# Optimization experiments

Measured on AMD Instinct MI355X. Metric: run time of the kernel, lower is better.

## Reference

```python
import jax, jax.numpy as jnp
import numpy as np

N_NODES = 50000
N_EDGES = 400000
F_IN = 128
HID = 64
HEADS = 8
N_CLASSES = 16
NEG_SLOPE = 0.2  # PyG GATConv default negative_slope


def _glorot(key, shape):
    fan_in, fan_out = shape[0], shape[-1]
    lim = jnp.sqrt(6.0 / (fan_in + fan_out))
    return jax.random.uniform(key, shape, jnp.float32, -lim, lim)


def setup_inputs() -> dict:
    key = jax.random.key(0)
    ks = jax.random.split(key, 16)
    x = jax.random.normal(ks[0], (N_NODES, F_IN), jnp.float32)
    edge_index = jax.random.randint(ks[1], (2, N_EDGES), 0, N_NODES, jnp.int64)
    # layer 0: F_IN -> HEADS*HID (concat)
    W0 = _glorot(ks[2], (F_IN, HEADS * HID))
    a_s0 = _glorot(ks[3], (HEADS, HID))
    a_d0 = _glorot(ks[4], (HEADS, HID))
    b0 = jnp.zeros((HEADS * HID,), jnp.float32)
    # layer 1: HEADS*HID -> HEADS*HID (concat)
    W1 = _glorot(ks[5], (HEADS * HID, HEADS * HID))
    a_s1 = _glorot(ks[6], (HEADS, HID))
    a_d1 = _glorot(ks[7], (HEADS, HID))
    b1 = jnp.zeros((HEADS * HID,), jnp.float32)
    # final layer: HEADS*HID -> N_CLASSES, heads=1, concat=False (mean over heads)
    W2 = _glorot(ks[8], (HEADS * HID, 1 * N_CLASSES))
    a_s2 = _glorot(ks[9], (1, N_CLASSES))
    a_d2 = _glorot(ks[10], (1, N_CLASSES))
    b2 = jnp.zeros((N_CLASSES,), jnp.float32)
    return {"x": x, "edge_index": edge_index,
            "W0": W0, "a_s0": a_s0, "a_d0": a_d0, "b0": b0,
            "W1": W1, "a_s1": a_s1, "a_d1": a_d1, "b1": b1,
            "W2": W2, "a_s2": a_s2, "a_d2": a_d2, "b2": b2}


def gat_conv(x, src, dst, W, a_src, a_dst, b, num_nodes, concat):
    """One PyG-style GATConv (self-loops already in src/dst).
    x: [N, F_in]; W: [F_in, H*C]; a_src/a_dst: [H, C]; b: [H*C] or [C]."""
    H, C = a_src.shape
    h = (x @ W).reshape(num_nodes, H, C)                    # [N,H,C]
    al_s = jnp.einsum('nhc,hc->nh', h, a_src)               # [N,H]
    al_d = jnp.einsum('nhc,hc->nh', h, a_dst)               # [N,H]
    e = jax.nn.leaky_relu(al_s[src] + al_d[dst], NEG_SLOPE) # [E,H]
    # scatter-softmax over incoming edges of each destination node
    m = jax.ops.segment_max(e, dst, num_segments=num_nodes)  # [N,H]
    ex = jnp.exp(e - m[dst])
    denom = jax.ops.segment_sum(ex, dst, num_segments=num_nodes)
    alpha = ex / denom[dst]                                  # [E,H]
    out = jax.ops.segment_sum(alpha[:, :, None] * h[src], dst,
                              num_segments=num_nodes)        # [N,H,C]
    if concat:
        return out.reshape(num_nodes, H * C) + b
    return out.mean(axis=1) + b


def reference(x, edge_index, W0, a_s0, a_d0, b0, W1, a_s1, a_d1, b1,
              W2, a_s2, a_d2, b2):
    N = x.shape[0]
    # PyG GATConv adds self-loops by default
    loops = jnp.arange(N, dtype=edge_index.dtype)
    src = jnp.concatenate([edge_index[0], loops])
    dst = jnp.concatenate([edge_index[1], loops])
    h = gat_conv(x, src, dst, W0, a_s0, a_d0, b0, N, concat=True)
    h = jax.nn.elu(h)  # dropout is identity in eval mode
    h = gat_conv(h, src, dst, W1, a_s1, a_d1, b1, N, concat=True)
    h = jax.nn.elu(h)
    return gat_conv(h, src, dst, W2, a_s2, a_d2, b2, N, concat=False)
```

## Files before the change

kernel.cpp:

```cpp
#include <hip/hip_runtime.h>

#define N_NODES 50000
#define N_EDGES 400000
#define E_TOT   450000
#define NEG 0.2f
#define NB_SCAN ((N_NODES + 255) / 256)
#define MAXD 64

typedef unsigned short ushort_t;
typedef __attribute__((ext_vector_type(8))) _Float16 half8;
typedef __attribute__((ext_vector_type(4))) float  f32x4;
typedef __attribute__((ext_vector_type(8))) unsigned short ushort8;

__device__ __forceinline__ ushort_t f2h(float f){
    _Float16 h = (_Float16)f;
    union { _Float16 h; ushort_t u; } v; v.h = h; return v.u;
}
__device__ __forceinline__ float h_lo(unsigned u){
    union { unsigned u; _Float16 h[2]; } v; v.u = u; return (float)v.h[0];
}
__device__ __forceinline__ float h_hi(unsigned u){
    union { unsigned u; _Float16 h[2]; } v; v.u = u; return (float)v.h[1];
}
__device__ __forceinline__ void gload_lds16(const void* g, void* l){
    __builtin_amdgcn_global_load_lds((const __attribute__((address_space(1))) void*)g,
                                     (__attribute__((address_space(3))) void*)l, 16, 0, 0);
}
__device__ __forceinline__ int wave_incl_scan(int v, int lane){
    #pragma unroll
    for(int off = 1; off < 64; off <<= 1){
        int t = __shfl_up(v, off, 64);
        if(lane >= off) v += t;
    }
    return v;
}


__global__ void count_deg(const int* __restrict__ ei, int* __restrict__ deg){
    int e = blockIdx.x*256 + threadIdx.x;
    if(e >= E_TOT) return;
    int dst = (e < N_EDGES) ? ei[N_EDGES + e] : (e - N_EDGES);
    atomicAdd(&deg[dst], 1);
}

__global__ void deg_block_sum(const int* __restrict__ deg, int* __restrict__ bsum){
    int i = blockIdx.x*256 + threadIdx.x;
    int lane = threadIdx.x & 63, wave = threadIdx.x >> 6;
    int v = (i < N_NODES) ? deg[i] : 0;
    #pragma unroll
    for(int off = 1; off < 64; off <<= 1) v += __shfl_xor(v, off, 64);
    __shared__ int sw[4];
    if(lane == 0) sw[wave] = v;
    __syncthreads();
    if(threadIdx.x == 0) bsum[blockIdx.x] = sw[0] + sw[1] + sw[2] + sw[3];
}

__global__ void scan_apply(const int* __restrict__ bsum,
                           int* __restrict__ dw, int* __restrict__ rowptr){
    __shared__ int soff;
    __shared__ int sw[4];
    int i = blockIdx.x*256 + threadIdx.x;
    int lane = threadIdx.x & 63, wave = threadIdx.x >> 6;
    if(wave == 0){
        int s = 0;
        for(int j = lane; j < (int)blockIdx.x; j += 64) s += bsum[j];
        #pragma unroll
        for(int off = 1; off < 64; off <<= 1) s += __shfl_xor(s, off, 64);
        if(lane == 0) soff = s;
    }
    int v = (i < N_NODES) ? dw[i] : 0;
    int incl = wave_incl_scan(v, lane);
    if(lane == 63) sw[wave] = incl;
    __syncthreads();
    int add = soff;
    for(int w = 0; w < wave; w++) add += sw[w];
    int excl = incl - v + add;
    if(i < N_NODES){ rowptr[i] = excl; dw[i] = excl; }
    if(i == N_NODES-1) rowptr[N_NODES] = excl + v;
}

__global__ void scatter_edges(const int* __restrict__ ei, int* __restrict__ wofs,
                              int* __restrict__ csr){
    int e = blockIdx.x*256 + threadIdx.x;
    if(e >= E_TOT) return;
    int src, dst;
    if(e < N_EDGES){ src = ei[e]; dst = ei[N_EDGES + e]; }
    else { src = dst = e - N_EDGES; }
    int pos = atomicAdd(&wofs[dst], 1);
    csr[pos] = src;
}


__global__ void cvt_all(const float* __restrict__ x, const float* __restrict__ W0,
                        const float* __restrict__ W1, const float* __restrict__ W2,
                        ushort_t* __restrict__ xbf, ushort_t* __restrict__ W0t,
                        ushort_t* __restrict__ W1t, ushort_t* __restrict__ W2t,
                        int* __restrict__ wofs){
    int i = blockIdx.x*256 + threadIdx.x;
    if(i < N_NODES*128) xbf[i] = f2h(x[i]);
    if(i < 512*128){ int n = i >> 7, k = i & 127; W0t[i] = f2h(W0[(size_t)k*512 + n]); }
    if(i < 512*512){ int n = i >> 9, k = i & 511; W1t[i] = f2h(W1[(size_t)k*512 + n]); }
    if(i < 16*512){ int n = i >> 9, k = i & 511; W2t[i] = f2h(W2[(size_t)k*16 + n]); }
    if(i < N_NODES) wofs[i] = 0;
}


template<int K>
__global__ __launch_bounds__(256) void gemm_bt(const ushort_t* __restrict__ A,
                                               const ushort_t* __restrict__ Bt,
                                               ushort_t* __restrict__ Cb,
                                               const float* __restrict__ a_s,
                                               const float* __restrict__ a_d,
                                               float* __restrict__ als,
                                               float* __restrict__ ald, int M){
    __shared__ ushort_t As[128*32];
    __shared__ ushort_t Bs[128*32];
    int tid  = threadIdx.x;
    int wave = tid >> 6, lane = tid & 63;
    int wm = wave & 1, wn = wave >> 1;
    int row0 = blockIdx.y * 128;
    int col0 = blockIdx.x * 128;

    f32x4 acc[4][4] = {};

    int lrow = lane >> 2;
    int lchk = (lane & 3) * 8;

    for(int kt = 0; kt < K; kt += 32){
        #pragma unroll
        for(int s = 0; s < 2; s++){
            int seg = wave*2 + s;
            int ar = row0 + seg*16 + lrow;
            ar = ar < M ? ar : M-1;
            gload_lds16(A  + (size_t)ar*K + kt + lchk, As + seg*512);
            int br = col0 + seg*16 + lrow;
            gload_lds16(Bt + (size_t)br*K + kt + lchk, Bs + seg*512);
        }
        __syncthreads();

        half8 a[4], b[4];
        int fm = lane & 15, fq = (lane >> 4) * 8;
        #pragma unroll
        for(int t = 0; t < 4; t++){
            a[t] = *(const half8*)&As[(wm*64 + t*16 + fm)*32 + fq];
            b[t] = *(const half8*)&Bs[(wn*64 + t*16 + fm)*32 + fq];
        }
        #pragma unroll
        for(int i = 0; i < 4; i++)
            #pragma unroll
            for(int j = 0; j < 4; j++)
                acc[i][j] = __builtin_amdgcn_mfma_f32_16x16x32_f16(a[i], b[j], acc[i][j], 0, 0, 0);
        __syncthreads();
    }

    int cm = (lane >> 4) * 4, cn = lane & 15;
    int head = (col0 + wn*64) >> 6;
    float as_[4], ad_[4];
    #pragma unroll
    for(int j = 0; j < 4; j++){
        int c = head*64 + cn + j*16;
        as_[j] = a_s[c]; ad_[j] = a_d[c];
    }
    #pragma unroll
    for(int i = 0; i < 4; i++){
        #pragma unroll
        for(int p = 0; p < 4; p++){
            int r = row0 + wm*64 + i*16 + cm + p;
            float ps = 0.f, pd = 0.f;
            if(r < M){
                ushort_t* cp = &Cb[(size_t)r*512 + col0 + wn*64 + cn];
                #pragma unroll
                for(int j = 0; j < 4; j++){
                    float v = acc[i][j][p];
                    cp[j*16] = f2h(v);
                    ps += v*as_[j]; pd += v*ad_[j];
                }
            }
            #pragma unroll
            for(int off = 1; off < 16; off <<= 1){
                ps += __shfl_xor(ps, off);
                pd += __shfl_xor(pd, off);
            }
            if(cn == 0 && r < M){ als[r*8 + head] = ps; ald[r*8 + head] = pd; }
        }
    }
}


__global__ __launch_bounds__(256, 4) void attn_agg(const ushort_t* __restrict__ h,
        const float* __restrict__ als, const float* __restrict__ ald,
        const int* __restrict__ rowptr, const int* __restrict__ csr,
        const float* __restrict__ bias, ushort_t* __restrict__ out){
    __shared__ float sm[4][8], sd[4][8];
    __shared__ float sex[4][MAXD][8];
    int wv = threadIdx.x >> 6, lane = threadIdx.x & 63;
    int n = blockIdx.x*4 + wv;
    int start = rowptr[n], end = rowptr[n+1];

    int cnt = end - start;
    int nmain = cnt < MAXD ? cnt : MAXD;
    int mend = start + nmain;
    int last = mend - 1;

    uint4 pp[8];
    #pragma unroll
    for(int k = 0; k < 8; k++){
        int j = start + k;
        int s = csr[j <= last ? j : last];
        pp[k] = *(const uint4*)&h[(size_t)s*512 + lane*8];
    }

    int hd = lane & 7, e8 = lane >> 3;
    float aldv = ald[n*8 + hd];
    float lmax = -1e30f;
    for(int idx = start + e8; idx < end; idx += 8){
        int e = idx - start;
        int src = csr[idx];
        float v = als[src*8 + hd] + aldv;
        v = v > 0.f ? v : NEG*v;
        if(e < MAXD) sex[wv][e][hd] = v;
        lmax = fmaxf(lmax, v);
    }
    for(int off = 8; off < 64; off <<= 1) lmax = fmaxf(lmax, __shfl_xor(lmax, off));
    float lsum = 0.f;
    for(int idx = start + e8; idx < end; idx += 8){
        int e = idx - start;
        float v;
        if(e < MAXD) v = sex[wv][e][hd];
        else { int src = csr[idx]; v = als[src*8 + hd] + aldv; v = v > 0.f ? v : NEG*v; }
        float ex = __expf(v - lmax);
        if(e < MAXD) sex[wv][e][hd] = ex;
        lsum += ex;
    }
    for(int off = 8; off < 64; off <<= 1) lsum += __shfl_xor(lsum, off);
    if(lane < 8){ sm[wv][hd] = lmax; sd[wv][hd] = 1.f / lsum; }
    __syncthreads();

    int head = lane >> 3;
    float inv = sd[wv][head];
    float acc[8] = {};

    int idx = start;
    for(;;){
        float ee[8];
        #pragma unroll
        for(int k = 0; k < 8; k++){
            int j = idx + k;
            ee[k] = (j < mend) ? sex[wv][j-start][head] : 0.f;
        }
        int nidx = idx + 8;
        bool more = nidx < mend;
        uint4 np[8];
        if(more){
            #pragma unroll
            for(int k = 0; k < 8; k++){
                int j = nidx + k;
                int s = csr[j <= last ? j : last];
                np[k] = *(const uint4*)&h[(size_t)s*512 + lane*8];
            }
        }
        #pragma unroll
        for(int k = 0; k < 8; k++){
            acc[0] += ee[k]*h_lo(pp[k].x); acc[1] += ee[k]*h_hi(pp[k].x);
            acc[2] += ee[k]*h_lo(pp[k].y); acc[3] += ee[k]*h_hi(pp[k].y);
            acc[4] += ee[k]*h_lo(pp[k].z); acc[5] += ee[k]*h_hi(pp[k].z);
            acc[6] += ee[k]*h_lo(pp[k].w); acc[7] += ee[k]*h_hi(pp[k].w);
        }
        if(!more) break;
        #pragma unroll
        for(int k = 0; k < 8; k++) pp[k] = np[k];
        idx = nidx;
    }

    if(mend < end){
        float m = sm[wv][head];
        float aldn = ald[n*8 + head];
        for(int ix = mend; ix < end; ix++){
            int src = csr[ix];
            float v = als[src*8 + head] + aldn;
            v = v > 0.f ? v : NEG*v;
            float e0 = __expf(v - m);
            uint4 p = *(const uint4*)&h[(size_t)src*512 + lane*8];
            acc[0] += e0*h_lo(p.x); acc[1] += e0*h_hi(p.x);
            acc[2] += e0*h_lo(p.y); acc[3] += e0*h_hi(p.y);
            acc[4] += e0*h_lo(p.z); acc[5] += e0*h_hi(p.z);
            acc[6] += e0*h_lo(p.w); acc[7] += e0*h_hi(p.w);
        }
    }

    ushort8 o;
    #pragma unroll
    for(int j = 0; j < 8; j++){
        float v = acc[j]*inv + bias[lane*8 + j];
        v = v > 0.f ? v : (__expf(v) - 1.f);
        o[j] = f2h(v);
    }
    *(ushort8*)&out[(size_t)n*512 + lane*8] = o;
}


__global__ __launch_bounds__(256) void gemm2_mfma(const ushort_t* __restrict__ A,
                                                  const ushort_t* __restrict__ W2t,
                                                  const float* __restrict__ a_s2,
                                                  const float* __restrict__ a_d2,
                                                  float* __restrict__ C,
                                                  float* __restrict__ als,
                                                  float* __restrict__ ald){
    int wave = threadIdx.x >> 6, lane = threadIdx.x & 63;
    long row0 = (long)(blockIdx.x*4 + wave)*16;
    int fr = lane & 15, fq = lane >> 4;
    long ar = row0 + fr;
    if(ar > N_NODES-1) ar = N_NODES-1;
    const ushort_t* ap = A + ar*512 + fq*8;
    const ushort_t* bp = W2t + (size_t)fr*512 + fq*8;
    f32x4 acc = {};
    #pragma unroll
    for(int kt = 0; kt < 512; kt += 32){
        half8 a = *(const half8*)(ap + kt);
        half8 b = *(const half8*)(bp + kt);
        acc = __builtin_amdgcn_mfma_f32_16x16x32_f16(a, b, acc, 0, 0, 0);
    }
    float as_ = a_s2[fr], ad_ = a_d2[fr];
    #pragma unroll
    for(int p = 0; p < 4; p++){
        long r = row0 + fq*4 + p;
        float v = acc[p];
        float ps = v*as_, pd = v*ad_;
        #pragma unroll
        for(int off = 1; off < 16; off <<= 1){
            ps += __shfl_xor(ps, off);
            pd += __shfl_xor(pd, off);
        }
        if(r < N_NODES){
            C[r*16 + fr] = v;
            if(fr == 0){ als[r] = ps; ald[r] = pd; }
        }
    }
}

__global__ __launch_bounds__(256) void attn_agg2(const float* __restrict__ h2,
        const float* __restrict__ als, const float* __restrict__ ald,
        const int* __restrict__ rowptr, const int* __restrict__ csr,
        const float* __restrict__ b2, float* __restrict__ out){
    __shared__ float sex2[16][MAXD+1];
    int wv = threadIdx.x >> 6, lane = threadIdx.x & 63;
    int q = lane >> 4, c = lane & 15;
    int slot = wv*4 + q;
    int n = blockIdx.x*16 + slot;
    int start = rowptr[n], end = rowptr[n+1];
    float aldv = ald[n];
    int cnt = end - start;
    int nmain = cnt < MAXD ? cnt : MAXD;
    int mend = start + nmain;

    float lmax = -1e30f;
    for(int idx = start + c; idx < end; idx += 16){
        int e = idx - start;
        float v = als[csr[idx]] + aldv; v = v > 0.f ? v : NEG*v;
        if(e < MAXD) sex2[slot][e] = v;
        lmax = fmaxf(lmax, v);
    }
    #pragma unroll
    for(int off = 1; off < 16; off <<= 1) lmax = fmaxf(lmax, __shfl_xor(lmax, off));
    float lsum = 0.f;
    for(int idx = start + c; idx < end; idx += 16){
        int e = idx - start;
        float v;
        if(e < MAXD) v = sex2[slot][e];
        else { v = als[csr[idx]] + aldv; v = v > 0.f ? v : NEG*v; }
        float ex = __expf(v - lmax);
        if(e < MAXD) sex2[slot][e] = ex;
        lsum += ex;
    }
    #pragma unroll
    for(int off = 1; off < 16; off <<= 1) lsum += __shfl_xor(lsum, off);
    float inv = 1.f / lsum;

    float acc = 0.f;
    for(int idx = start; idx < mend; idx++){
        int src = csr[idx];
        float ex = sex2[slot][idx - start];
        acc += ex * h2[(size_t)src*16 + c];
    }
    for(int idx = mend; idx < end; idx++){
        int src = csr[idx];
        float v = als[src] + aldv; v = v > 0.f ? v : NEG*v;
        acc += __expf(v - lmax) * h2[(size_t)src*16 + c];
    }
    out[(size_t)n*16 + c] = acc*inv + b2[c];
}


extern "C" void kernel_launch(void* const* d_in, const int* in_sizes, int n_in,
                              void* d_out, int out_size, void* d_ws, size_t ws_size,
                              hipStream_t stream) {
    const float* x    = (const float*)d_in[0];
    const int*   ei   = (const int*)  d_in[1];
    const float* W0   = (const float*)d_in[2];
    const float* a_s0 = (const float*)d_in[3];
    const float* a_d0 = (const float*)d_in[4];
    const float* b0   = (const float*)d_in[5];
    const float* W1   = (const float*)d_in[6];
    const float* a_s1 = (const float*)d_in[7];
    const float* a_d1 = (const float*)d_in[8];
    const float* b1   = (const float*)d_in[9];
    const float* W2   = (const float*)d_in[10];
    const float* a_s2 = (const float*)d_in[11];
    const float* a_d2 = (const float*)d_in[12];
    const float* b2   = (const float*)d_in[13];
    float* out = (float*)d_out;

    char* w = (char*)d_ws;
    auto alloc = [&](size_t bytes){ void* p = (void*)w; w += (bytes + 255) & ~(size_t)255; return p; };
    int*      rowptr = (int*)     alloc((N_NODES+1)*sizeof(int));
    int*      wofs   = (int*)     alloc(N_NODES*sizeof(int));
    int*      bsum   = (int*)     alloc(NB_SCAN*sizeof(int));
    int*      csr    = (int*)     alloc(E_TOT*sizeof(int));
    float*    als    = (float*)   alloc((size_t)N_NODES*8*sizeof(float));
    float*    ald    = (float*)   alloc((size_t)N_NODES*8*sizeof(float));
    ushort_t* hb     = (ushort_t*)alloc((size_t)N_NODES*512*sizeof(ushort_t));
    ushort_t* hbf    = (ushort_t*)alloc((size_t)N_NODES*512*sizeof(ushort_t));
    ushort_t* xbf    = (ushort_t*)alloc((size_t)N_NODES*128*sizeof(ushort_t));
    ushort_t* W0t    = (ushort_t*)alloc((size_t)512*128*sizeof(ushort_t));
    ushort_t* W1t    = (ushort_t*)alloc((size_t)512*512*sizeof(ushort_t));
    ushort_t* W2t    = (ushort_t*)alloc((size_t)16*512*sizeof(ushort_t));
    float*    h2     = (float*)   alloc((size_t)N_NODES*16*sizeof(float));

    cvt_all<<<(N_NODES*128+255)/256, 256, 0, stream>>>(x, W0, W1, W2, xbf, W0t, W1t, W2t, wofs);

    count_deg<<<(E_TOT+255)/256, 256, 0, stream>>>(ei, wofs);
    deg_block_sum<<<NB_SCAN, 256, 0, stream>>>(wofs, bsum);
    scan_apply<<<NB_SCAN, 256, 0, stream>>>(bsum, wofs, rowptr);
    scatter_edges<<<(E_TOT+255)/256, 256, 0, stream>>>(ei, wofs, csr);

    gemm_bt<128><<<dim3(4, (N_NODES+127)/128), 256, 0, stream>>>(xbf, W0t, hb, a_s0, a_d0, als, ald, N_NODES);
    attn_agg<<<N_NODES/4, 256, 0, stream>>>(hb, als, ald, rowptr, csr, b0, hbf);

    gemm_bt<512><<<dim3(4, (N_NODES+127)/128), 256, 0, stream>>>(hbf, W1t, hb, a_s1, a_d1, als, ald, N_NODES);
    attn_agg<<<N_NODES/4, 256, 0, stream>>>(hb, als, ald, rowptr, csr, b1, hbf);

    gemm2_mfma<<<(N_NODES+63)/64, 256, 0, stream>>>(hbf, W2t, a_s2, a_d2, h2, als, ald);
    attn_agg2<<<N_NODES/16, 256, 0, stream>>>(h2, als, ald, rowptr, csr, b2, out);
}
```

Before: 451.4 us.

## Add 256x256-tile 8-wave GEMM for layer 1 and simplify attn_agg gather loop

Adds a new 512-thread GEMM kernel with 256x256 output tiles, a double-buffered 128KB dynamic LDS staging area, swizzled LDS layout and s_setprio around MFMA, and uses it for the layer-1 512x512 projection. The goal is more operand reuse and fewer blocks than the 128x128 template. Separately, attn_agg drops its software-pipelined prefetch of the next 8 neighbor rows in favour of a simple per-iteration load, and its launch bounds no longer request 4 blocks per CU. Register pressure may fall, but gather latency is no longer hidden across iterations.

```diff
diff --git a/kernel.cpp b/kernel.cpp
--- a/kernel.cpp
+++ b/kernel.cpp
@@ -187,7 +187,117 @@
 }
 
 
-__global__ __launch_bounds__(256, 4) void attn_agg(const ushort_t* __restrict__ h,
+__global__ __launch_bounds__(512, 2) void gemm_bt8(const ushort_t* __restrict__ A,
+                                                   const ushort_t* __restrict__ Bt,
+                                                   ushort_t* __restrict__ Cb,
+                                                   const float* __restrict__ a_s,
+                                                   const float* __restrict__ a_d,
+                                                   float* __restrict__ als,
+                                                   float* __restrict__ ald, int M){
+    extern __shared__ ushort_t lds[];
+    const int K = 512;
+    int tid = threadIdx.x, wave = tid >> 6, lane = tid & 63;
+    int wm = wave >> 2, wn = wave & 3;
+    int row0 = blockIdx.y * 256;
+    int col0 = blockIdx.x * 256;
+
+    int lr = lane >> 3;
+    int cs8 = ((lane & 7) ^ lr) << 3;
+    int arows[4], brows[4];
+    #pragma unroll
+    for(int i = 0; i < 4; i++){
+        int r = row0 + (wave << 5) + (i << 3) + lr;
+        arows[i] = r < M ? r : M-1;
+        brows[i] = col0 + (wave << 5) + (i << 3) + lr;
+    }
+
+    int l15 = lane & 15, fq = lane >> 4;
+    int xr = (lane & 7) << 4;
+    int xco0 = ((fq << 4)      ) ^ xr;
+    int xco1 = (64 | (fq << 4)) ^ xr;
+
+    f32x4 acc[8][4] = {};
+
+    auto stage = [&](int nb, int kt, int i){
+        ushort_t* la = lds + nb*16384 + (wave << 11) + (i << 9);
+        ushort_t* lb = lds + 32768 + nb*16384 + (wave << 11) + (i << 9);
+        gload_lds16(A  + (size_t)arows[i]*K + kt + cs8, la);
+        gload_lds16(Bt + (size_t)brows[i]*K + kt + cs8, lb);
+    };
+
+    #pragma unroll
+    for(int i = 0; i < 4; i++) stage(0, 0, i);
+
+    for(int it = 0; it < 8; ++it){
+        int b = it & 1;
+        asm volatile("s_waitcnt vmcnt(0)" ::: "memory");
+        __builtin_amdgcn_s_barrier();
+        const char* Ac = (const char*)(lds + b*16384);
+        const char* Bc = (const char*)(lds + 32768 + b*16384);
+        #pragma unroll
+        for(int p = 0; p < 4; ++p){
+            if(it < 7) stage(b ^ 1, (it + 1) << 6, p);
+            half8 aF[2][2], bF[4][2];
+            #pragma unroll
+            for(int m2 = 0; m2 < 2; m2++){
+                int ro = (((wm << 7) + (((p << 1) | m2) << 4) + l15)) << 7;
+                aF[m2][0] = *(const half8*)(Ac + ro + xco0);
+                aF[m2][1] = *(const half8*)(Ac + ro + xco1);
+            }
+            #pragma unroll
+            for(int nj = 0; nj < 4; nj++){
+                int ro = (((wn << 6) + (nj << 4) + l15)) << 7;
+                bF[nj][0] = *(const half8*)(Bc + ro + xco0);
+                bF[nj][1] = *(const half8*)(Bc + ro + xco1);
+            }
+            __builtin_amdgcn_s_barrier();
+            __builtin_amdgcn_s_setprio(1);
+            #pragma unroll
+            for(int m2 = 0; m2 < 2; m2++)
+                #pragma unroll
+                for(int nj = 0; nj < 4; nj++){
+                    acc[(p<<1)|m2][nj] = __builtin_amdgcn_mfma_f32_16x16x32_f16(aF[m2][0], bF[nj][0], acc[(p<<1)|m2][nj], 0, 0, 0);
+                    acc[(p<<1)|m2][nj] = __builtin_amdgcn_mfma_f32_16x16x32_f16(aF[m2][1], bF[nj][1], acc[(p<<1)|m2][nj], 0, 0, 0);
+                }
+            __builtin_amdgcn_s_setprio(0);
+            __builtin_amdgcn_s_barrier();
+        }
+    }
+
+    int head = (col0 >> 6) + wn;
+    float asv[4], adv[4];
+    #pragma unroll
+    for(int nj = 0; nj < 4; nj++){
+        int c = (head << 6) + (nj << 4) + l15;
+        asv[nj] = a_s[c]; adv[nj] = a_d[c];
+    }
+    #pragma unroll
+    for(int mi = 0; mi < 8; mi++){
+        #pragma unroll
+        for(int p2 = 0; p2 < 4; p2++){
+            int r = row0 + (wm << 7) + (mi << 4) + (fq << 2) + p2;
+            float ps = 0.f, pd = 0.f;
+            if(r < M){
+                ushort_t* cp = &Cb[(size_t)r*512 + (head << 6) + l15];
+                #pragma unroll
+                for(int nj = 0; nj < 4; nj++){
+                    float v = acc[mi][nj][p2];
+                    cp[nj << 4] = f2h(v);
+                    ps += v*asv[nj]; pd += v*adv[nj];
+                }
+            }
+            #pragma unroll
+            for(int off = 1; off < 16; off <<= 1){
+                ps += __shfl_xor(ps, off);
+                pd += __shfl_xor(pd, off);
+            }
+            if(l15 == 0 && r < M){ als[r*8 + head] = ps; ald[r*8 + head] = pd; }
+        }
+    }
+}
+
+
+__global__ __launch_bounds__(256) void attn_agg(const ushort_t* __restrict__ h,
         const float* __restrict__ als, const float* __restrict__ ald,
         const int* __restrict__ rowptr, const int* __restrict__ csr,
         const float* __restrict__ bias, ushort_t* __restrict__ out){
@@ -196,19 +306,6 @@
     int wv = threadIdx.x >> 6, lane = threadIdx.x & 63;
     int n = blockIdx.x*4 + wv;
     int start = rowptr[n], end = rowptr[n+1];
-
-    int cnt = end - start;
-    int nmain = cnt < MAXD ? cnt : MAXD;
-    int mend = start + nmain;
-    int last = mend - 1;
-
-    uint4 pp[8];
-    #pragma unroll
-    for(int k = 0; k < 8; k++){
-        int j = start + k;
-        int s = csr[j <= last ? j : last];
-        pp[k] = *(const uint4*)&h[(size_t)s*512 + lane*8];
-    }
 
     int hd = lane & 7, e8 = lane >> 3;
     float aldv = ald[n*8 + hd];
@@ -240,24 +337,24 @@
     float inv = sd[wv][head];
     float acc[8] = {};
 
-    int idx = start;
-    for(;;){
-        float ee[8];
+    int cnt = end - start;
+    int nmain = cnt < MAXD ? cnt : MAXD;
+    int mend = start + nmain;
+    int last = mend - 1;
+    for(int idx = start; idx < mend; idx += 8){
+        int ss[8]; uint4 pp[8]; float ee[8];
+        #pragma unroll
+        for(int k = 0; k < 8; k++){
+            int j = idx + k;
+            ss[k] = csr[j <= last ? j : last];
+        }
+        #pragma unroll
+        for(int k = 0; k < 8; k++)
+            pp[k] = *(const uint4*)&h[(size_t)ss[k]*512 + lane*8];
         #pragma unroll
         for(int k = 0; k < 8; k++){
             int j = idx + k;
             ee[k] = (j < mend) ? sex[wv][j-start][head] : 0.f;
-        }
-        int nidx = idx + 8;
-        bool more = nidx < mend;
-        uint4 np[8];
-        if(more){
-            #pragma unroll
-            for(int k = 0; k < 8; k++){
-                int j = nidx + k;
-                int s = csr[j <= last ? j : last];
-                np[k] = *(const uint4*)&h[(size_t)s*512 + lane*8];
-            }
         }
         #pragma unroll
         for(int k = 0; k < 8; k++){
@@ -266,17 +363,12 @@
             acc[4] += ee[k]*h_lo(pp[k].z); acc[5] += ee[k]*h_hi(pp[k].z);
             acc[6] += ee[k]*h_lo(pp[k].w); acc[7] += ee[k]*h_hi(pp[k].w);
         }
-        if(!more) break;
-        #pragma unroll
-        for(int k = 0; k < 8; k++) pp[k] = np[k];
-        idx = nidx;
-    }
-
+    }
     if(mend < end){
         float m = sm[wv][head];
         float aldn = ald[n*8 + head];
-        for(int ix = mend; ix < end; ix++){
-            int src = csr[ix];
+        for(int idx = mend; idx < end; idx++){
+            int src = csr[idx];
             float v = als[src*8 + head] + aldn;
             v = v > 0.f ? v : NEG*v;
             float e0 = __expf(v - m);
@@ -426,6 +518,9 @@
     ushort_t* W2t    = (ushort_t*)alloc((size_t)16*512*sizeof(ushort_t));
     float*    h2     = (float*)   alloc((size_t)N_NODES*16*sizeof(float));
 
+    (void)hipFuncSetAttribute((const void*)gemm_bt8,
+                              hipFuncAttributeMaxDynamicSharedMemorySize, 131072);
+
     cvt_all<<<(N_NODES*128+255)/256, 256, 0, stream>>>(x, W0, W1, W2, xbf, W0t, W1t, W2t, wofs);
 
     count_deg<<<(E_TOT+255)/256, 256, 0, stream>>>(ei, wofs);
@@ -436,7 +531,7 @@
     gemm_bt<128><<<dim3(4, (N_NODES+127)/128), 256, 0, stream>>>(xbf, W0t, hb, a_s0, a_d0, als, ald, N_NODES);
     attn_agg<<<N_NODES/4, 256, 0, stream>>>(hb, als, ald, rowptr, csr, b0, hbf);
 
-    gemm_bt<512><<<dim3(4, (N_NODES+127)/128), 256, 0, stream>>>(hbf, W1t, hb, a_s1, a_d1, als, ald, N_NODES);
+    gemm_bt8<<<dim3(2, (N_NODES+255)/256), 512, 131072, stream>>>(hbf, W1t, hb, a_s1, a_d1, als, ald, N_NODES);
     attn_agg<<<N_NODES/4, 256, 0, stream>>>(hb, als, ald, rowptr, csr, b1, hbf);
 
     gemm2_mfma<<<(N_NODES+63)/64, 256, 0, stream>>>(hbf, W2t, a_s2, a_d2, h2, als, ald);
```

After: 426.6 us. 1.06x faster.
